# Kernel optimization log

Measured on AMD Instinct MI355X. Metric: run time of the kernel, lower is better.

The kernel has to match this reference:

```python
import jax, jax.numpy as jnp
import numpy as np


def setup_inputs() -> dict:
    key = jax.random.key(0)
    ks = jax.random.split(key, 7)
    N, C_in, H, W = 32, 512, 56, 56
    C_sq, C_e1, C_e3 = 64, 256, 256
    return {
        "x": jax.random.normal(ks[0], (N, C_in, H, W), dtype=jnp.float32),
        "squeeze_w": jax.random.normal(ks[1], (C_sq, C_in), dtype=jnp.float32) * 0.05,
        "squeeze_b": jax.random.normal(ks[2], (C_sq,), dtype=jnp.float32) * 0.05,
        "expand1x1_w": jax.random.normal(ks[3], (C_e1, C_sq), dtype=jnp.float32) * 0.05,
        "expand1x1_b": jax.random.normal(ks[4], (C_e1,), dtype=jnp.float32) * 0.05,
        "expand3x3_w": jax.random.normal(ks[5], (C_e3, C_sq, 3, 3), dtype=jnp.float32) * 0.05,
        "expand3x3_b": jax.random.normal(ks[6], (C_e3,), dtype=jnp.float32) * 0.05,
    }


def reference(x, squeeze_w, squeeze_b, expand1x1_w, expand1x1_b, expand3x3_w, expand3x3_b):
    # Squeeze 1x1 conv + ReLU: [N,C_in,H,W] -> [N,C_sq,H,W]
    s = jax.nn.relu(
        jnp.einsum("oc,nchw->nohw", squeeze_w, x) + squeeze_b[None, :, None, None]
    )
    # Expand 1x1 branch + ReLU
    e1 = jax.nn.relu(
        jnp.einsum("oc,nchw->nohw", expand1x1_w, s) + expand1x1_b[None, :, None, None]
    )
    # Expand 3x3 branch (padding=1) + ReLU
    e3 = jax.lax.conv_general_dilated(
        s, expand3x3_w,
        window_strides=(1, 1), padding=((1, 1), (1, 1)),
        dimension_numbers=("NCHW", "OIHW", "NCHW"),
    )
    e3 = jax.nn.relu(e3 + expand3x3_b[None, :, None, None])
    # Channel concat: expand1x1 first, expand3x3 second
    return jnp.concatenate([e1, e3], axis=1)
```

## Files before the change

kernel.cpp:

```cpp
#include <hip/hip_runtime.h>
#include <cstdint>
#include <cstddef>


typedef _Float16 f16;
typedef __attribute__((ext_vector_type(8))) _Float16 f16x8;
typedef __attribute__((ext_vector_type(4))) _Float16 f16x4;
typedef __attribute__((ext_vector_type(4))) float    f32x4;

#define MFMA(a, b, c) __builtin_amdgcn_mfma_f32_16x16x32_f16((a), (b), (c), 0, 0, 0)

#define NIMG 32
#define CIN  512
#define HW   3136
#define W56  56
#define CSQ  64
#define CE   256

__global__ __launch_bounds__(256) void fire_prep(
    const float* __restrict__ sw, const float* __restrict__ e1w,
    const float* __restrict__ e3w,
    f16* __restrict__ Wsq, f16* __restrict__ W1, f16* __restrict__ W3)
{
    int t = blockIdx.x * 256 + threadIdx.x;
    if (t < CSQ * CIN) {
        Wsq[t] = (f16)sw[t];
    } else if (t < CSQ * CIN + CE * CSQ) {
        int j = t - CSQ * CIN;
        W1[j] = (f16)e1w[j];
    } else {
        int j = t - (CSQ * CIN + CE * CSQ);
        if (j < 9 * CE * CSQ) {
            int tap = j >> 14;
            int rem = j & 16383;
            int o = rem >> 6;
            int i = rem & 63;
            W3[j] = (f16)e3w[(o * CSQ + i) * 9 + tap];
        }
    }
}

__global__ __launch_bounds__(256) void fire_squeeze2(
    const float* __restrict__ x, const float* __restrict__ sb,
    const f16* __restrict__ Wsq, f16* __restrict__ Sws)
{
    const int tid  = threadIdx.x;
    const int lane = tid & 63, wv = tid >> 6;
    const int i = lane & 15, g = lane >> 4;
    const int w  = blockIdx.x * 4 + wv;
    const int n  = w / 49;
    const int p0 = (w % 49) * 64;

    const float* xp = x + (size_t)n * CIN * HW + p0 + 4 * i;

    f32x4 acc[4][4] = {};
    #pragma unroll
    for (int kk = 0; kk < 16; ++kk) {
        const int k0 = kk * 32 + g * 8;
        f16x8 b[4];
        #pragma unroll
        for (int v = 0; v < 8; ++v) {
            float4 q = *(const float4*)(xp + (size_t)(k0 + v) * HW);
            b[0][v] = (f16)q.x;
            b[1][v] = (f16)q.y;
            b[2][v] = (f16)q.z;
            b[3][v] = (f16)q.w;
        }
        #pragma unroll
        for (int m = 0; m < 4; ++m) {
            f16x8 a = *(const f16x8*)(Wsq + (16 * m + i) * CIN + k0);
            #pragma unroll
            for (int c = 0; c < 4; ++c)
                acc[m][c] = MFMA(a, b[c], acc[m][c]);
        }
    }

    #pragma unroll
    for (int m = 0; m < 4; ++m) {
        const int oc = 16 * m + 4 * g;
        const float4 bb = *(const float4*)(sb + oc);
        #pragma unroll
        for (int c = 0; c < 4; ++c) {
            const int px = p0 + 4 * i + c;
            f16x4 st;
            st[0] = (f16)fmaxf(acc[m][c][0] + bb.x, 0.f);
            st[1] = (f16)fmaxf(acc[m][c][1] + bb.y, 0.f);
            st[2] = (f16)fmaxf(acc[m][c][2] + bb.z, 0.f);
            st[3] = (f16)fmaxf(acc[m][c][3] + bb.w, 0.f);
            *(f16x4*)(Sws + ((size_t)n * HW + px) * CSQ + oc) = st;
        }
    }
}

__global__ __launch_bounds__(256) void fire_expand1(
    const f16* __restrict__ Sws, const f16* __restrict__ W1,
    const float* __restrict__ b1, float* __restrict__ out)
{
    const int tid  = threadIdx.x;
    const int lane = tid & 63, wv = tid >> 6;
    const int i = lane & 15, g = lane >> 4;
    const int n  = blockIdx.y;
    const int p0 = blockIdx.x * 64;

    f32x4 acc[4][4] = {};
    #pragma unroll
    for (int kk = 0; kk < 2; ++kk) {
        const int k0 = kk * 32 + g * 8;
        f16x8 b[4];
        #pragma unroll
        for (int c = 0; c < 4; ++c)
            b[c] = *(const f16x8*)(Sws + ((size_t)n * HW + p0 + 16 * c + i) * CSQ + k0);
        #pragma unroll
        for (int m = 0; m < 4; ++m) {
            f16x8 a = *(const f16x8*)(W1 + (64 * wv + 16 * m + i) * CSQ + k0);
            #pragma unroll
            for (int c = 0; c < 4; ++c)
                acc[m][c] = MFMA(a, b[c], acc[m][c]);
        }
    }

    #pragma unroll
    for (int m = 0; m < 4; ++m) {
        const int oc = 64 * wv + 16 * m + 4 * g;
        const float4 bb = *(const float4*)(b1 + oc);
        #pragma unroll
        for (int c = 0; c < 4; ++c) {
            float* op = out + ((size_t)n * 512 + oc) * HW + p0 + 16 * c + i;
            op[0 * (size_t)HW] = fmaxf(acc[m][c][0] + bb.x, 0.f);
            op[1 * (size_t)HW] = fmaxf(acc[m][c][1] + bb.y, 0.f);
            op[2 * (size_t)HW] = fmaxf(acc[m][c][2] + bb.z, 0.f);
            op[3 * (size_t)HW] = fmaxf(acc[m][c][3] + bb.w, 0.f);
        }
    }
}

__global__ __launch_bounds__(256) void fire_expand3(
    const f16* __restrict__ Sws, const f16* __restrict__ W3,
    const float* __restrict__ b3, float* __restrict__ out)
{
    __shared__ f16 Slds[4 * 58 * 64];

    const int tid  = threadIdx.x;
    const int lane = tid & 63, wv = tid >> 6;
    const int i = lane & 15, g = lane >> 4;
    const int n  = blockIdx.y;
    const int rb = blockIdx.x;
    const int r0 = rb * 2;

    #pragma unroll
    for (int it = 0; it < 8; ++it) {
        int task = it * 256 + tid;
        if (task < 232 * 8) {
            int s  = task >> 3, ck = task & 7;
            int tr = s / 58,   tc = s % 58;
            int h = r0 - 1 + tr, w = tc - 1;
            int4 val = make_int4(0, 0, 0, 0);
            if (h >= 0 && h < W56 && w >= 0 && w < W56)
                val = *(const int4*)(Sws + ((size_t)n * HW + h * W56 + w) * CSQ + ck * 8);
            int off = s * 128 + ck * 16;
            off ^= ((s & 7) << 4);
            *(int4*)((char*)Slds + off) = val;
        }
    }
    __syncthreads();

    int q0[7];
    #pragma unroll
    for (int c = 0; c < 7; ++c) {
        int pl  = 16 * c + i;
        int r   = (pl >= W56) ? 1 : 0;
        int col = pl - r * W56;
        q0[c] = r * 58 + col;
    }

    f32x4 acc[4][7] = {};
    for (int dh = 0; dh < 3; ++dh) {
        for (int dw = 0; dw < 3; ++dw) {
            const f16* wtap = W3 + (size_t)(dh * 3 + dw) * CE * CSQ;
            const int toff = dh * 58 + dw;
            #pragma unroll
            for (int kk = 0; kk < 2; ++kk) {
                const int k0 = kk * 32 + g * 8;
                f16x8 b[7];
                #pragma unroll
                for (int c = 0; c < 7; ++c) {
                    int q   = q0[c] + toff;
                    int off = q * 128 + kk * 64 + g * 16;
                    off ^= ((q & 7) << 4);
                    b[c] = *(const f16x8*)((const char*)Slds + off);
                }
                #pragma unroll
                for (int m = 0; m < 4; ++m) {
                    f16x8 a = *(const f16x8*)(wtap + (64 * wv + 16 * m + i) * CSQ + k0);
                    #pragma unroll
                    for (int c = 0; c < 7; ++c)
                        acc[m][c] = MFMA(a, b[c], acc[m][c]);
                }
            }
        }
    }

    #pragma unroll
    for (int m = 0; m < 4; ++m) {
        const int ocl = 64 * wv + 16 * m + 4 * g;
        const float4 bb = *(const float4*)(b3 + ocl);
        #pragma unroll
        for (int c = 0; c < 7; ++c) {
            float* op = out + ((size_t)n * 512 + 256 + ocl) * HW + rb * 112 + 16 * c + i;
            op[0 * (size_t)HW] = fmaxf(acc[m][c][0] + bb.x, 0.f);
            op[1 * (size_t)HW] = fmaxf(acc[m][c][1] + bb.y, 0.f);
            op[2 * (size_t)HW] = fmaxf(acc[m][c][2] + bb.z, 0.f);
            op[3 * (size_t)HW] = fmaxf(acc[m][c][3] + bb.w, 0.f);
        }
    }
}

extern "C" void kernel_launch(void* const* d_in, const int* in_sizes, int n_in,
                              void* d_out, int out_size, void* d_ws, size_t ws_size,
                              hipStream_t stream)
{
    const float* x  = (const float*)d_in[0];
    const float* sw = (const float*)d_in[1];
    const float* sb = (const float*)d_in[2];
    const float* w1 = (const float*)d_in[3];
    const float* b1 = (const float*)d_in[4];
    const float* w3 = (const float*)d_in[5];
    const float* b3 = (const float*)d_in[6];
    float* out = (float*)d_out;

    f16* Sws = (f16*)d_ws;
    f16* Wsq = Sws + (size_t)NIMG * HW * CSQ;
    f16* W1b = Wsq + CSQ * CIN;
    f16* W3b = W1b + CE * CSQ;

    fire_prep<<<768, 256, 0, stream>>>(sw, w1, w3, Wsq, W1b, W3b);
    fire_squeeze2<<<392, 256, 0, stream>>>(x, sb, Wsq, Sws);
    fire_expand1<<<dim3(49, 32), 256, 0, stream>>>(Sws, W1b, b1, out);
    fire_expand3<<<dim3(28, 32), 256, 0, stream>>>(Sws, W3b, b3, out);
}
```

Measured before the change: 175.1 us.

## Fuse squeeze, expand1x1 and expand3x3 into one kernel with LDS-resident squeeze tile

Merges the three conv kernels into one. Each block computes the squeeze output for its two rows plus a one-row halo directly into LDS, then runs both expand branches from that tile. This removes the global write and re-read of the f16 squeeze intermediate and two kernel launches. The cost is recomputing halo rows (up to double the squeeze work, which reads x over 512 channels) and a longer serial per-block pipeline with fewer blocks for the squeeze phase.

After: 377.9 us. 116% more time.

```diff
diff --git a/kernel.cpp b/kernel.cpp
--- a/kernel.cpp
+++ b/kernel.cpp
@@ -16,6 +16,10 @@
 #define W56  56
 #define CSQ  64
 #define CE   256
+
+__device__ __forceinline__ int sw_off(int q, int bc) {
+    return (q * 128 + bc) ^ ((q & 7) << 4);
+}
 
 __global__ __launch_bounds__(256) void fire_prep(
     const float* __restrict__ sw, const float* __restrict__ e1w,
@@ -40,102 +44,10 @@
     }
 }
 
-__global__ __launch_bounds__(256) void fire_squeeze2(
-    const float* __restrict__ x, const float* __restrict__ sb,
-    const f16* __restrict__ Wsq, f16* __restrict__ Sws)
-{
-    const int tid  = threadIdx.x;
-    const int lane = tid & 63, wv = tid >> 6;
-    const int i = lane & 15, g = lane >> 4;
-    const int w  = blockIdx.x * 4 + wv;
-    const int n  = w / 49;
-    const int p0 = (w % 49) * 64;
-
-    const float* xp = x + (size_t)n * CIN * HW + p0 + 4 * i;
-
-    f32x4 acc[4][4] = {};
-    #pragma unroll
-    for (int kk = 0; kk < 16; ++kk) {
-        const int k0 = kk * 32 + g * 8;
-        f16x8 b[4];
-        #pragma unroll
-        for (int v = 0; v < 8; ++v) {
-            float4 q = *(const float4*)(xp + (size_t)(k0 + v) * HW);
-            b[0][v] = (f16)q.x;
-            b[1][v] = (f16)q.y;
-            b[2][v] = (f16)q.z;
-            b[3][v] = (f16)q.w;
-        }
-        #pragma unroll
-        for (int m = 0; m < 4; ++m) {
-            f16x8 a = *(const f16x8*)(Wsq + (16 * m + i) * CIN + k0);
-            #pragma unroll
-            for (int c = 0; c < 4; ++c)
-                acc[m][c] = MFMA(a, b[c], acc[m][c]);
-        }
-    }
-
-    #pragma unroll
-    for (int m = 0; m < 4; ++m) {
-        const int oc = 16 * m + 4 * g;
-        const float4 bb = *(const float4*)(sb + oc);
-        #pragma unroll
-        for (int c = 0; c < 4; ++c) {
-            const int px = p0 + 4 * i + c;
-            f16x4 st;
-            st[0] = (f16)fmaxf(acc[m][c][0] + bb.x, 0.f);
-            st[1] = (f16)fmaxf(acc[m][c][1] + bb.y, 0.f);
-            st[2] = (f16)fmaxf(acc[m][c][2] + bb.z, 0.f);
-            st[3] = (f16)fmaxf(acc[m][c][3] + bb.w, 0.f);
-            *(f16x4*)(Sws + ((size_t)n * HW + px) * CSQ + oc) = st;
-        }
-    }
-}
-
-__global__ __launch_bounds__(256) void fire_expand1(
-    const f16* __restrict__ Sws, const f16* __restrict__ W1,
-    const float* __restrict__ b1, float* __restrict__ out)
-{
-    const int tid  = threadIdx.x;
-    const int lane = tid & 63, wv = tid >> 6;
-    const int i = lane & 15, g = lane >> 4;
-    const int n  = blockIdx.y;
-    const int p0 = blockIdx.x * 64;
-
-    f32x4 acc[4][4] = {};
-    #pragma unroll
-    for (int kk = 0; kk < 2; ++kk) {
-        const int k0 = kk * 32 + g * 8;
-        f16x8 b[4];
-        #pragma unroll
-        for (int c = 0; c < 4; ++c)
-            b[c] = *(const f16x8*)(Sws + ((size_t)n * HW + p0 + 16 * c + i) * CSQ + k0);
-        #pragma unroll
-        for (int m = 0; m < 4; ++m) {
-            f16x8 a = *(const f16x8*)(W1 + (64 * wv + 16 * m + i) * CSQ + k0);
-            #pragma unroll
-            for (int c = 0; c < 4; ++c)
-                acc[m][c] = MFMA(a, b[c], acc[m][c]);
-        }
-    }
-
-    #pragma unroll
-    for (int m = 0; m < 4; ++m) {
-        const int oc = 64 * wv + 16 * m + 4 * g;
-        const float4 bb = *(const float4*)(b1 + oc);
-        #pragma unroll
-        for (int c = 0; c < 4; ++c) {
-            float* op = out + ((size_t)n * 512 + oc) * HW + p0 + 16 * c + i;
-            op[0 * (size_t)HW] = fmaxf(acc[m][c][0] + bb.x, 0.f);
-            op[1 * (size_t)HW] = fmaxf(acc[m][c][1] + bb.y, 0.f);
-            op[2 * (size_t)HW] = fmaxf(acc[m][c][2] + bb.z, 0.f);
-            op[3 * (size_t)HW] = fmaxf(acc[m][c][3] + bb.w, 0.f);
-        }
-    }
-}
-
-__global__ __launch_bounds__(256) void fire_expand3(
-    const f16* __restrict__ Sws, const f16* __restrict__ W3,
+__global__ __launch_bounds__(256) void fire_fused(
+    const float* __restrict__ x,  const float* __restrict__ sb,
+    const f16* __restrict__ Wsq,  const f16* __restrict__ W1,
+    const float* __restrict__ b1, const f16* __restrict__ W3,
     const float* __restrict__ b3, float* __restrict__ out)
 {
     __shared__ f16 Slds[4 * 58 * 64];
@@ -147,19 +59,69 @@
     const int rb = blockIdx.x;
     const int r0 = rb * 2;
 
-    #pragma unroll
-    for (int it = 0; it < 8; ++it) {
-        int task = it * 256 + tid;
-        if (task < 232 * 8) {
-            int s  = task >> 3, ck = task & 7;
-            int tr = s / 58,   tc = s % 58;
-            int h = r0 - 1 + tr, w = tc - 1;
-            int4 val = make_int4(0, 0, 0, 0);
-            if (h >= 0 && h < W56 && w >= 0 && w < W56)
-                val = *(const int4*)(Sws + ((size_t)n * HW + h * W56 + w) * CSQ + ck * 8);
-            int off = s * 128 + ck * 16;
-            off ^= ((s & 7) << 4);
-            *(int4*)((char*)Slds + off) = val;
+    const int vr_start = (r0 == 0) ? 0 : (r0 - 1);
+    const int vr_end   = (r0 + 2 < W56) ? (r0 + 2) : (W56 - 1);
+    const int nr       = vr_end - vr_start + 1;
+    const int nvalid   = nr * W56;
+    const int t_base   = vr_start - (r0 - 1);
+
+    {
+        int4* p = (int4*)Slds;
+        #pragma unroll
+        for (int t = 0; t < 8; ++t) {
+            int idx = t * 256 + tid;
+            if (idx < 1856) p[idx] = make_int4(0, 0, 0, 0);
+        }
+    }
+    __syncthreads();
+
+    {
+        const int  pxl0 = wv * 64 + 4 * i;
+        const bool ldv  = (pxl0 < nvalid);
+        const float* xp = x + (size_t)n * CIN * HW + vr_start * W56 + pxl0;
+
+        if (wv * 64 < nvalid) {
+            f32x4 acc[4][4] = {};
+            for (int kk = 0; kk < 16; ++kk) {
+                const int k0 = kk * 32 + g * 8;
+                f16x8 b[4];
+                #pragma unroll
+                for (int v = 0; v < 8; ++v) {
+                    float4 q = make_float4(0.f, 0.f, 0.f, 0.f);
+                    if (ldv) q = *(const float4*)(xp + (size_t)(k0 + v) * HW);
+                    b[0][v] = (f16)q.x;
+                    b[1][v] = (f16)q.y;
+                    b[2][v] = (f16)q.z;
+                    b[3][v] = (f16)q.w;
+                }
+                #pragma unroll
+                for (int m = 0; m < 4; ++m) {
+                    f16x8 a = *(const f16x8*)(Wsq + (16 * m + i) * CIN + k0);
+                    #pragma unroll
+                    for (int c = 0; c < 4; ++c)
+                        acc[m][c] = MFMA(a, b[c], acc[m][c]);
+                }
+            }
+            if (ldv) {
+                #pragma unroll
+                for (int m = 0; m < 4; ++m) {
+                    const int oc = 16 * m + 4 * g;
+                    const float4 bb = *(const float4*)(sb + oc);
+                    #pragma unroll
+                    for (int c = 0; c < 4; ++c) {
+                        const int pxl = pxl0 + c;
+                        const int hl  = pxl / W56;
+                        const int col = pxl - hl * W56;
+                        const int q   = (t_base + hl) * 58 + col + 1;
+                        f16x4 st;
+                        st[0] = (f16)fmaxf(acc[m][c][0] + bb.x, 0.f);
+                        st[1] = (f16)fmaxf(acc[m][c][1] + bb.y, 0.f);
+                        st[2] = (f16)fmaxf(acc[m][c][2] + bb.z, 0.f);
+                        st[3] = (f16)fmaxf(acc[m][c][3] + bb.w, 0.f);
+                        *(f16x4*)((char*)Slds + sw_off(q, oc * 2)) = st;
+                    }
+                }
+            }
         }
     }
     __syncthreads();
@@ -173,44 +135,77 @@
         q0[c] = r * 58 + col;
     }
 
-    f32x4 acc[4][7] = {};
-    for (int dh = 0; dh < 3; ++dh) {
-        for (int dw = 0; dw < 3; ++dw) {
-            const f16* wtap = W3 + (size_t)(dh * 3 + dw) * CE * CSQ;
-            const int toff = dh * 58 + dw;
-            #pragma unroll
-            for (int kk = 0; kk < 2; ++kk) {
-                const int k0 = kk * 32 + g * 8;
-                f16x8 b[7];
-                #pragma unroll
-                for (int c = 0; c < 7; ++c) {
-                    int q   = q0[c] + toff;
-                    int off = q * 128 + kk * 64 + g * 16;
-                    off ^= ((q & 7) << 4);
-                    b[c] = *(const f16x8*)((const char*)Slds + off);
-                }
-                #pragma unroll
-                for (int m = 0; m < 4; ++m) {
-                    f16x8 a = *(const f16x8*)(wtap + (64 * wv + 16 * m + i) * CSQ + k0);
-                    #pragma unroll
-                    for (int c = 0; c < 7; ++c)
-                        acc[m][c] = MFMA(a, b[c], acc[m][c]);
-                }
-            }
-        }
-    }
-
-    #pragma unroll
-    for (int m = 0; m < 4; ++m) {
-        const int ocl = 64 * wv + 16 * m + 4 * g;
-        const float4 bb = *(const float4*)(b3 + ocl);
-        #pragma unroll
-        for (int c = 0; c < 7; ++c) {
-            float* op = out + ((size_t)n * 512 + 256 + ocl) * HW + rb * 112 + 16 * c + i;
-            op[0 * (size_t)HW] = fmaxf(acc[m][c][0] + bb.x, 0.f);
-            op[1 * (size_t)HW] = fmaxf(acc[m][c][1] + bb.y, 0.f);
-            op[2 * (size_t)HW] = fmaxf(acc[m][c][2] + bb.z, 0.f);
-            op[3 * (size_t)HW] = fmaxf(acc[m][c][3] + bb.w, 0.f);
+    {
+        f32x4 acc[4][7] = {};
+        #pragma unroll
+        for (int kk = 0; kk < 2; ++kk) {
+            const int k0 = kk * 32 + g * 8;
+            f16x8 b[7];
+            #pragma unroll
+            for (int c = 0; c < 7; ++c) {
+                int q = q0[c] + 59;
+                b[c] = *(const f16x8*)((const char*)Slds + sw_off(q, kk * 64 + g * 16));
+            }
+            #pragma unroll
+            for (int m = 0; m < 4; ++m) {
+                f16x8 a = *(const f16x8*)(W1 + (64 * wv + 16 * m + i) * CSQ + k0);
+                #pragma unroll
+                for (int c = 0; c < 7; ++c)
+                    acc[m][c] = MFMA(a, b[c], acc[m][c]);
+            }
+        }
+        #pragma unroll
+        for (int m = 0; m < 4; ++m) {
+            const int oc = 64 * wv + 16 * m + 4 * g;
+            const float4 bb = *(const float4*)(b1 + oc);
+            #pragma unroll
+            for (int c = 0; c < 7; ++c) {
+                float* op = out + ((size_t)n * 512 + oc) * HW + rb * 112 + 16 * c + i;
+                op[0 * (size_t)HW] = fmaxf(acc[m][c][0] + bb.x, 0.f);
+                op[1 * (size_t)HW] = fmaxf(acc[m][c][1] + bb.y, 0.f);
+                op[2 * (size_t)HW] = fmaxf(acc[m][c][2] + bb.z, 0.f);
+                op[3 * (size_t)HW] = fmaxf(acc[m][c][3] + bb.w, 0.f);
+            }
+        }
+    }
+
+    {
+        f32x4 acc[4][7] = {};
+        for (int dh = 0; dh < 3; ++dh) {
+            for (int dw = 0; dw < 3; ++dw) {
+                const f16* wtap = W3 + (size_t)(dh * 3 + dw) * CE * CSQ;
+                const int toff = dh * 58 + dw;
+                #pragma unroll
+                for (int kk = 0; kk < 2; ++kk) {
+                    const int k0 = kk * 32 + g * 8;
+                    f16x8 b[7];
+                    #pragma unroll
+                    for (int c = 0; c < 7; ++c) {
+                        int q = q0[c] + toff;
+                        b[c] = *(const f16x8*)((const char*)Slds + sw_off(q, kk * 64 + g * 16));
+                    }
+                    #pragma unroll
+                    for (int m = 0; m < 4; ++m) {
+                        f16x8 a = *(const f16x8*)(wtap + (64 * wv + 16 * m + i) * CSQ + k0);
+                        #pragma unroll
+                        for (int c = 0; c < 7; ++c)
+                            acc[m][c] = MFMA(a, b[c], acc[m][c]);
+                    }
+                }
+            }
+        }
+        #pragma unroll
+        for (int m = 0; m < 4; ++m) {
+            const int ocl = 64 * wv + 16 * m + 4 * g;
+            const float4 bb = *(const float4*)(b3 + ocl);
+            #pragma unroll
+            for (int c = 0; c < 7; ++c) {
+                float* op = out + ((size_t)n * 512 + 256 + ocl) * HW + rb * 112 + 16 * c + i;
+                op[0 * (size_t)HW] = fmaxf(acc[m][c][0] + bb.x, 0.f);
+                op[1 * (size_t)HW] = fmaxf(acc[m][c][1] + bb.y, 0.f);
+                op[2 * (size_t)HW] = fmaxf(acc[m][c][2] + bb.z, 0.f);
+                op[3 * (size_t)HW] = fmaxf(acc[m][c][3] + bb.w, 0.f);
+            }
         }
     }
 }
@@ -228,13 +223,10 @@
     const float* b3 = (const float*)d_in[6];
     float* out = (float*)d_out;
 
-    f16* Sws = (f16*)d_ws;
-    f16* Wsq = Sws + (size_t)NIMG * HW * CSQ;
+    f16* Wsq = (f16*)d_ws;
     f16* W1b = Wsq + CSQ * CIN;
     f16* W3b = W1b + CE * CSQ;
 
     fire_prep<<<768, 256, 0, stream>>>(sw, w1, w3, Wsq, W1b, W3b);
-    fire_squeeze2<<<392, 256, 0, stream>>>(x, sb, Wsq, Sws);
-    fire_expand1<<<dim3(49, 32), 256, 0, stream>>>(Sws, W1b, b1, out);
-    fire_expand3<<<dim3(28, 32), 256, 0, stream>>>(Sws, W3b, b3, out);
-}
+    fire_fused<<<dim3(28, 32), 256, 0, stream>>>(x, sb, Wsq, W1b, b1, W3b, b3, out);
+}
```

## Stage expand outputs through LDS for coalesced stores; split squeeze into single-wave blocks

Applied to the files above, without the earlier changes.

Both expand kernels now write their ReLU'd accumulator tiles into a padded per-wave LDS buffer. They then store each output-channel row with consecutive lanes writing consecutive pixels, replacing the old scattered 16-lane strided stores into NCHW output. The squeeze kernel moves from four-wave blocks to single-wave blocks with four times as many blocks, giving finer scheduling across CUs. The cost is extra LDS traffic and capacity, which may lower occupancy in expand3.

New measurement: 190.5 us. 1.09x slower.

```diff
diff --git a/kernel.cpp b/kernel.cpp
--- a/kernel.cpp
+++ b/kernel.cpp
@@ -40,14 +40,13 @@
     }
 }
 
-__global__ __launch_bounds__(256) void fire_squeeze2(
+__global__ __launch_bounds__(64) void fire_squeeze3(
     const float* __restrict__ x, const float* __restrict__ sb,
     const f16* __restrict__ Wsq, f16* __restrict__ Sws)
 {
-    const int tid  = threadIdx.x;
-    const int lane = tid & 63, wv = tid >> 6;
+    const int lane = threadIdx.x;
     const int i = lane & 15, g = lane >> 4;
-    const int w  = blockIdx.x * 4 + wv;
+    const int w  = blockIdx.x;
     const int n  = w / 49;
     const int p0 = (w % 49) * 64;
 
@@ -92,10 +91,12 @@
     }
 }
 
-__global__ __launch_bounds__(256) void fire_expand1(
+__global__ __launch_bounds__(256) void fire_expand1t(
     const f16* __restrict__ Sws, const f16* __restrict__ W1,
     const float* __restrict__ b1, float* __restrict__ out)
 {
+    __shared__ float T[4][16 * 65];
+
     const int tid  = threadIdx.x;
     const int lane = tid & 63, wv = tid >> 6;
     const int i = lane & 15, g = lane >> 4;
@@ -119,26 +120,31 @@
         }
     }
 
+    float* Tw = T[wv];
     #pragma unroll
     for (int m = 0; m < 4; ++m) {
-        const int oc = 64 * wv + 16 * m + 4 * g;
-        const float4 bb = *(const float4*)(b1 + oc);
-        #pragma unroll
-        for (int c = 0; c < 4; ++c) {
-            float* op = out + ((size_t)n * 512 + oc) * HW + p0 + 16 * c + i;
-            op[0 * (size_t)HW] = fmaxf(acc[m][c][0] + bb.x, 0.f);
-            op[1 * (size_t)HW] = fmaxf(acc[m][c][1] + bb.y, 0.f);
-            op[2 * (size_t)HW] = fmaxf(acc[m][c][2] + bb.z, 0.f);
-            op[3 * (size_t)HW] = fmaxf(acc[m][c][3] + bb.w, 0.f);
-        }
-    }
-}
-
-__global__ __launch_bounds__(256) void fire_expand3(
+        const int oc0 = 64 * wv + 16 * m;
+        const float4 bb = *(const float4*)(b1 + oc0 + 4 * g);
+        const float bbv[4] = {bb.x, bb.y, bb.z, bb.w};
+        #pragma unroll
+        for (int c = 0; c < 4; ++c)
+            #pragma unroll
+            for (int v = 0; v < 4; ++v)
+                Tw[(4 * g + v) * 65 + 16 * c + i] = fmaxf(acc[m][c][v] + bbv[v], 0.f);
+        #pragma unroll
+        for (int r = 0; r < 16; ++r) {
+            float val = Tw[r * 65 + lane];
+            out[((size_t)n * 512 + oc0 + r) * HW + p0 + lane] = val;
+        }
+    }
+}
+
+__global__ __launch_bounds__(256) void fire_expand3t(
     const f16* __restrict__ Sws, const f16* __restrict__ W3,
     const float* __restrict__ b3, float* __restrict__ out)
 {
-    __shared__ f16 Slds[4 * 58 * 64];
+    __shared__ f16   Slds[4 * 58 * 64];
+    __shared__ float T3[4][16 * 113];
 
     const int tid  = threadIdx.x;
     const int lane = tid & 63, wv = tid >> 6;
@@ -185,8 +191,7 @@
                 #pragma unroll
                 for (int c = 0; c < 7; ++c) {
                     int q   = q0[c] + toff;
-                    int off = q * 128 + kk * 64 + g * 16;
-                    off ^= ((q & 7) << 4);
+                    int off = (q * 128 + kk * 64 + g * 16) ^ ((q & 7) << 4);
                     b[c] = *(const f16x8*)((const char*)Slds + off);
                 }
                 #pragma unroll
@@ -200,17 +205,22 @@
         }
     }
 
+    float* Tw = T3[wv];
     #pragma unroll
     for (int m = 0; m < 4; ++m) {
-        const int ocl = 64 * wv + 16 * m + 4 * g;
-        const float4 bb = *(const float4*)(b3 + ocl);
-        #pragma unroll
-        for (int c = 0; c < 7; ++c) {
-            float* op = out + ((size_t)n * 512 + 256 + ocl) * HW + rb * 112 + 16 * c + i;
-            op[0 * (size_t)HW] = fmaxf(acc[m][c][0] + bb.x, 0.f);
-            op[1 * (size_t)HW] = fmaxf(acc[m][c][1] + bb.y, 0.f);
-            op[2 * (size_t)HW] = fmaxf(acc[m][c][2] + bb.z, 0.f);
-            op[3 * (size_t)HW] = fmaxf(acc[m][c][3] + bb.w, 0.f);
+        const int oc0 = 64 * wv + 16 * m;
+        const float4 bb = *(const float4*)(b3 + oc0 + 4 * g);
+        const float bbv[4] = {bb.x, bb.y, bb.z, bb.w};
+        #pragma unroll
+        for (int c = 0; c < 7; ++c)
+            #pragma unroll
+            for (int v = 0; v < 4; ++v)
+                Tw[(4 * g + v) * 113 + 16 * c + i] = fmaxf(acc[m][c][v] + bbv[v], 0.f);
+        #pragma unroll
+        for (int r = 0; r < 16; ++r) {
+            float* op = out + ((size_t)n * 512 + 256 + oc0 + r) * HW + rb * 112;
+            op[lane] = Tw[r * 113 + lane];
+            if (lane < 48) op[64 + lane] = Tw[r * 113 + 64 + lane];
         }
     }
 }
@@ -234,7 +244,7 @@
     f16* W3b = W1b + CE * CSQ;
 
     fire_prep<<<768, 256, 0, stream>>>(sw, w1, w3, Wsq, W1b, W3b);
-    fire_squeeze2<<<392, 256, 0, stream>>>(x, sb, Wsq, Sws);
-    fire_expand1<<<dim3(49, 32), 256, 0, stream>>>(Sws, W1b, b1, out);
-    fire_expand3<<<dim3(28, 32), 256, 0, stream>>>(Sws, W3b, b3, out);
-}
+    fire_squeeze3<<<1568, 64, 0, stream>>>(x, sb, Wsq, Sws);
+    fire_expand1t<<<dim3(49, 32), 256, 0, stream>>>(Sws, W1b, b1, out);
+    fire_expand3t<<<dim3(28, 32), 256, 0, stream>>>(Sws, W3b, b3, out);
+}
```

## Restructure expand1x1 to stage outputs in LDS for coalesced row stores

Applied to the files above, without the earlier changes.

The expand1x1 kernel is reorganized so each block handles 16 output channels of one image, and each wave loops over 64-pixel chunks. Results are transposed through a per-wave LDS tile so each output row of 64 contiguous pixels is written with fully coalesced stores, instead of the previous scattered 16-wide strided stores. The cost is that the squeeze activations are re-read 16 times per image (once per channel group) rather than once. The grid also shrinks to 512 blocks.

Result: slower. 180.9 us (+3.3%).

```diff
diff --git a/kernel.cpp b/kernel.cpp
--- a/kernel.cpp
+++ b/kernel.cpp
@@ -92,44 +92,55 @@
     }
 }
 
-__global__ __launch_bounds__(256) void fire_expand1(
+__global__ __launch_bounds__(256) void fire_expand1s(
     const f16* __restrict__ Sws, const f16* __restrict__ W1,
     const float* __restrict__ b1, float* __restrict__ out)
 {
+    __shared__ float T[4][16 * 68];
+
     const int tid  = threadIdx.x;
     const int lane = tid & 63, wv = tid >> 6;
     const int i = lane & 15, g = lane >> 4;
+    const int cg = blockIdx.x;
     const int n  = blockIdx.y;
-    const int p0 = blockIdx.x * 64;
-
-    f32x4 acc[4][4] = {};
-    #pragma unroll
-    for (int kk = 0; kk < 2; ++kk) {
-        const int k0 = kk * 32 + g * 8;
-        f16x8 b[4];
+    const int oc0 = cg * 16;
+
+    f16x8 a0 = *(const f16x8*)(W1 + (oc0 + i) * CSQ + 0  + g * 8);
+    f16x8 a1 = *(const f16x8*)(W1 + (oc0 + i) * CSQ + 32 + g * 8);
+
+    const float bias = b1[oc0 + (lane >> 2)];
+    const float4 bb = *(const float4*)(b1 + oc0 + 4 * g);
+    const float bbv[4] = {bb.x, bb.y, bb.z, bb.w};
+    (void)bias;
+
+    const f16* Sn = Sws + (size_t)n * HW * CSQ;
+    float* Tw = T[wv];
+
+    for (int it = 0; it < 13; ++it) {
+        const int cc = wv + 4 * it;
+        if (cc >= 49) break;
+        const int p0 = cc * 64;
+
+        f32x4 acc[4] = {};
+        #pragma unroll
+        for (int c = 0; c < 4; ++c) {
+            const f16* sp = Sn + (size_t)(p0 + 16 * c + i) * CSQ + g * 8;
+            f16x8 b0 = *(const f16x8*)(sp);
+            f16x8 b1f = *(const f16x8*)(sp + 32);
+            acc[c] = MFMA(a0, b0, acc[c]);
+            acc[c] = MFMA(a1, b1f, acc[c]);
+        }
+
         #pragma unroll
         for (int c = 0; c < 4; ++c)
-            b[c] = *(const f16x8*)(Sws + ((size_t)n * HW + p0 + 16 * c + i) * CSQ + k0);
-        #pragma unroll
-        for (int m = 0; m < 4; ++m) {
-            f16x8 a = *(const f16x8*)(W1 + (64 * wv + 16 * m + i) * CSQ + k0);
             #pragma unroll
-            for (int c = 0; c < 4; ++c)
-                acc[m][c] = MFMA(a, b[c], acc[m][c]);
-        }
-    }
-
-    #pragma unroll
-    for (int m = 0; m < 4; ++m) {
-        const int oc = 64 * wv + 16 * m + 4 * g;
-        const float4 bb = *(const float4*)(b1 + oc);
-        #pragma unroll
-        for (int c = 0; c < 4; ++c) {
-            float* op = out + ((size_t)n * 512 + oc) * HW + p0 + 16 * c + i;
-            op[0 * (size_t)HW] = fmaxf(acc[m][c][0] + bb.x, 0.f);
-            op[1 * (size_t)HW] = fmaxf(acc[m][c][1] + bb.y, 0.f);
-            op[2 * (size_t)HW] = fmaxf(acc[m][c][2] + bb.z, 0.f);
-            op[3 * (size_t)HW] = fmaxf(acc[m][c][3] + bb.w, 0.f);
+            for (int v = 0; v < 4; ++v)
+                Tw[(4 * g + v) * 68 + 16 * c + i] = fmaxf(acc[c][v] + bbv[v], 0.f);
+
+        #pragma unroll
+        for (int r = 0; r < 16; ++r) {
+            float val = Tw[r * 68 + lane];
+            out[((size_t)n * 512 + oc0 + r) * HW + p0 + lane] = val;
         }
     }
 }
@@ -185,8 +196,7 @@
                 #pragma unroll
                 for (int c = 0; c < 7; ++c) {
                     int q   = q0[c] + toff;
-                    int off = q * 128 + kk * 64 + g * 16;
-                    off ^= ((q & 7) << 4);
+                    int off = (q * 128 + kk * 64 + g * 16) ^ ((q & 7) << 4);
                     b[c] = *(const f16x8*)((const char*)Slds + off);
                 }
                 #pragma unroll
@@ -235,6 +245,6 @@
 
     fire_prep<<<768, 256, 0, stream>>>(sw, w1, w3, Wsq, W1b, W3b);
     fire_squeeze2<<<392, 256, 0, stream>>>(x, sb, Wsq, Sws);
-    fire_expand1<<<dim3(49, 32), 256, 0, stream>>>(Sws, W1b, b1, out);
+    fire_expand1s<<<dim3(16, 32), 256, 0, stream>>>(Sws, W1b, b1, out);
     fire_expand3<<<dim3(28, 32), 256, 0, stream>>>(Sws, W3b, b3, out);
 }
```
